# Optimization experiments

Measured on AMD Instinct MI355X. Metric: run time of the kernel, lower is better.

The kernel has to match this reference:

```python
import jax, jax.numpy as jnp
import numpy as np

B, S, D = 8, 1024, 2048
H, HD = 16, 128          # n_heads, head_dim (H*HD == D)
ROPE = 64                # rotary dims per head (front slice)
MAXB, MAXS = 10, 1024    # kv-cache buffer sizes (hardcoded in module)
START_POS = 0


def _apply_rope(x, cos_half, sin_half):
    # x: (BH, S, ROPE); cos/sin_half: (S, ROPE//2) -> tiled to (S, ROPE)
    cos_full = jnp.concatenate([cos_half, cos_half], axis=-1)
    sin_full = jnp.concatenate([sin_half, sin_half], axis=-1)
    half = x.shape[-1] // 2
    x1, x2 = x[..., :half], x[..., half:]
    rotated = jnp.concatenate([-x2, x1], axis=-1)
    return x * cos_full + rotated * sin_full


def setup_inputs() -> dict:
    key = jax.random.key(0)
    ks = jax.random.split(key, 6)
    sc = 0.02
    x = jax.random.normal(ks[0], (B, S, D), dtype=jnp.float32)
    wq = jax.random.normal(ks[1], (D, D), dtype=jnp.float32) * sc
    wk = jax.random.normal(ks[2], (D, D), dtype=jnp.float32) * sc
    wv = jax.random.normal(ks[3], (D, D), dtype=jnp.float32) * sc
    wo = jax.random.normal(ks[4], (D, D), dtype=jnp.float32) * sc
    bq = jnp.zeros((D,), jnp.float32)
    bk = jnp.zeros((D,), jnp.float32)
    bv = jnp.zeros((D,), jnp.float32)
    bo = jnp.zeros((D,), jnp.float32)
    # RoPE tables (HF "half" layout): angles over positions
    half = ROPE // 2
    inv_freq = 1.0 / (10000.0 ** (jnp.arange(half, dtype=jnp.float32) / half))
    ang = jnp.arange(S, dtype=jnp.float32)[:, None] * inv_freq[None, :]  # (S, half)
    cos_half = jnp.cos(ang)
    sin_half = jnp.sin(ang)
    mask = jnp.zeros((S, S), jnp.float32)  # additive mask, (seq, end_pos)
    cache_k = jnp.zeros((MAXB, MAXS, H * HD), jnp.float32)
    cache_v = jnp.zeros((MAXB, MAXS, H * HD), jnp.float32)
    return {
        "x": x, "wq": wq, "bq": bq, "wk": wk, "bk": bk, "wv": wv, "bv": bv,
        "wo": wo, "bo": bo, "cos_half": cos_half, "sin_half": sin_half,
        "mask": mask, "cache_k": cache_k, "cache_v": cache_v,
        "start_pos": START_POS,
    }


def reference(x, wq, bq, wk, bk, wv, bv, wo, bo, cos_half, sin_half, mask,
              cache_k, cache_v, start_pos):
    b, s, _ = x.shape
    end_pos = start_pos + s
    # QKV projections (torch Linear: y = x @ W.T + b)
    q = (x @ wq.T + bq).reshape(b, s, H, HD)
    k = (x @ wk.T + bk).reshape(b, s, H, HD)
    v = (x @ wv.T + bv).reshape(b, s, H, HD)
    # Partial RoPE on the first ROPE dims of each head
    q_head = q[..., :ROPE].transpose(0, 2, 1, 3).reshape(b * H, s, ROPE)
    k_head = k[..., :ROPE].transpose(0, 2, 1, 3).reshape(b * H, s, ROPE)
    q_head = _apply_rope(q_head, cos_half, sin_half)
    k_head = _apply_rope(k_head, cos_half, sin_half)
    q_head = q_head.reshape(b, H, s, ROPE).transpose(0, 2, 1, 3)
    k_head = k_head.reshape(b, H, s, ROPE).transpose(0, 2, 1, 3)
    q = jnp.concatenate([q_head, q[..., ROPE:]], axis=-1)
    k = jnp.concatenate([k_head, k[..., ROPE:]], axis=-1)
    # KV-cache write then read (start_pos is a static python int)
    cache_k = jax.lax.dynamic_update_slice(cache_k, k.reshape(b, s, H * HD), (0, start_pos, 0))
    cache_v = jax.lax.dynamic_update_slice(cache_v, v.reshape(b, s, H * HD), (0, start_pos, 0))
    k_cached = cache_k[:b, :end_pos].reshape(b, end_pos, H, HD)
    v_cached = cache_v[:b, :end_pos].reshape(b, end_pos, H, HD)
    # Unnormalized attention: no softmax, no scaling
    scores = jnp.einsum('bshd,bthd->bsht', q, k_cached)  # (B,S,H,T)
    scores = scores + mask[:, None, :]                   # (S,1,T) broadcast
    a_sum = jnp.einsum('bsht,bthd->bshd', scores, v_cached)
    out = a_sum.reshape(b, s, H * HD) @ wo.T + bo
    return out
```

## Files before the change

kernel.cpp:

```cpp
#include <hip/hip_runtime.h>
#include <stdint.h>

#define B_ 8
#define S_ 1024
#define D_ 2048
#define H_ 16
#define HD_ 128
#define NROW 8192
#define NQKV 6144

typedef __bf16 bf16;
typedef bf16  bf16x8 __attribute__((ext_vector_type(8)));
typedef bf16  bf16x4 __attribute__((ext_vector_type(4)));
typedef float f32x4  __attribute__((ext_vector_type(4)));

#define AS1 __attribute__((address_space(1)))
#define AS3 __attribute__((address_space(3)))

__device__ __forceinline__ void gl_lds16(const bf16* g, bf16* l) {
  __builtin_amdgcn_global_load_lds((AS1 void*)g, (AS3 void*)l, 16, 0, 0);
}

__global__ __launch_bounds__(256) void prep(const float* __restrict__ x,
                                            const float* __restrict__ wq,
                                            const float* __restrict__ wk,
                                            const float* __restrict__ wv,
                                            const float* __restrict__ wo,
                                            const float* __restrict__ mask,
                                            const float* __restrict__ bq,
                                            const float* __restrict__ bk,
                                            const float* __restrict__ bv,
                                            bf16* __restrict__ xb,
                                            bf16* __restrict__ wqkvb,
                                            bf16* __restrict__ wob,
                                            bf16* __restrict__ maskb,
                                            float* __restrict__ bqkv) {
  long i = (long)blockIdx.x * 256 + threadIdx.x;
  if (i < 8650752) {
    const float* src; bf16* dst; long j;
    if (i < 4194304)      { src = x;    dst = xb;              j = i; }
    else if (i < 5242880) { src = wq;   dst = wqkvb;           j = i - 4194304; }
    else if (i < 6291456) { src = wk;   dst = wqkvb + 4194304; j = i - 5242880; }
    else if (i < 7340032) { src = wv;   dst = wqkvb + 8388608; j = i - 6291456; }
    else if (i < 8388608) { src = wo;   dst = wob;             j = i - 7340032; }
    else                  { src = mask; dst = maskb;           j = i - 8388608; }
    float4 v = reinterpret_cast<const float4*>(src)[j];
    bf16x4 o;
    o.x = (bf16)v.x; o.y = (bf16)v.y; o.z = (bf16)v.z; o.w = (bf16)v.w;
    reinterpret_cast<bf16x4*>(dst)[j] = o;
  } else {
    long e = (i - 8650752) * 4;
    const float* s = (e < 2048) ? bq + e : (e < 4096 ? bk + (e - 2048) : bv + (e - 4096));
    *reinterpret_cast<float4*>(bqkv + e) = *reinterpret_cast<const float4*>(s);
  }
}

#define READ_A4(QA, KS, Ab)                                                   \
  _Pragma("unroll") for (int mi = 0; mi < 4; mi++)                            \
    af[mi] = *reinterpret_cast<const bf16x8*>(                                \
        (Ab) + aoff + ((((QA)*4 + mi)*2) + (KS))*512);

#define READ_B4(KS, Bb)                                                       \
  _Pragma("unroll") for (int ni = 0; ni < 4; ni++)                            \
    bfr[ni] = *reinterpret_cast<const bf16x8*>(                               \
        (Bb) + boff + ((ni*2) + (KS))*512);

#define MFMA16(QA)                                                            \
  _Pragma("unroll") for (int mi = 0; mi < 4; mi++)                            \
  _Pragma("unroll") for (int ni = 0; ni < 4; ni++)                            \
    acc[(QA)*4 + mi][ni] = __builtin_amdgcn_mfma_f32_16x16x32_bf16(           \
        af[mi], bfr[ni], acc[(QA)*4 + mi][ni], 0, 0, 0);

#define STAGE_H0(An, Bn, koff)                                                \
  gl_lds16(agA + (koff),           (An) + wid*1024);                          \
  gl_lds16(agA + 128*la + (koff),  (An) + (wid + 8)*1024);                    \
  gl_lds16(agB + (koff),           (Bn) + wid*1024);                          \
  gl_lds16(agB + 128*lb + (koff),  (Bn) + (wid + 8)*1024);

#define STAGE_H1(An, Bn, koff)                                                \
  gl_lds16(agA + (koff) + 32,          (An) + wid*1024 + 512);                \
  gl_lds16(agA + 128*la + (koff) + 32, (An) + (wid + 8)*1024 + 512);          \
  gl_lds16(agB + (koff) + 32,          (Bn) + wid*1024 + 512);                \
  gl_lds16(agB + 128*lb + (koff) + 32, (Bn) + (wid + 8)*1024 + 512);

#define GEMM256_MAIN_LOOP(NT)                                                 \
  { bf16* An = lds; bf16* Bn = lds + 16384;                                   \
    STAGE_H0(An, Bn, 0); STAGE_H1(An, Bn, 0); }                               \
  for (int t = 0; t < (NT); ++t) {                                            \
    const bf16* Ab = lds + (t & 1) * 32768;                                   \
    const bf16* Bb = Ab + 16384;                                              \
    bf16* An = lds + ((t & 1) ^ 1) * 32768;                                   \
    bf16* Bn = An + 16384;                                                    \
    const long kn = (long)(t + 1) * 64;                                       \
    const bool pf = (t + 1) < (NT);                                           \
    bf16x8 af[4], bfr[4];                                                     \
    asm volatile("s_waitcnt vmcnt(4)" ::: "memory");                          \
    __builtin_amdgcn_s_barrier();                                             \
    READ_A4(0, 0, Ab); READ_B4(0, Bb);                                        \
    if (pf) { STAGE_H0(An, Bn, kn); }                                         \
    asm volatile("s_waitcnt lgkmcnt(0)" ::: "memory");                        \
    __builtin_amdgcn_sched_barrier(0);                                        \
    __builtin_amdgcn_s_setprio(1); MFMA16(0); __builtin_amdgcn_s_setprio(0);  \
    READ_A4(1, 0, Ab);                                                        \
    asm volatile("s_waitcnt lgkmcnt(0)" ::: "memory");                        \
    __builtin_amdgcn_sched_barrier(0);                                        \
    __builtin_amdgcn_s_setprio(1); MFMA16(1); __builtin_amdgcn_s_setprio(0);  \
    if (pf) asm volatile("s_waitcnt vmcnt(4)" ::: "memory");                  \
    else    asm volatile("s_waitcnt vmcnt(0)" ::: "memory");                  \
    __builtin_amdgcn_s_barrier();                                             \
    READ_A4(0, 1, Ab); READ_B4(1, Bb);                                        \
    if (pf) { STAGE_H1(An, Bn, kn); }                                         \
    asm volatile("s_waitcnt lgkmcnt(0)" ::: "memory");                        \
    __builtin_amdgcn_sched_barrier(0);                                        \
    __builtin_amdgcn_s_setprio(1); MFMA16(0); __builtin_amdgcn_s_setprio(0);  \
    READ_A4(1, 1, Ab);                                                        \
    asm volatile("s_waitcnt lgkmcnt(0)" ::: "memory");                        \
    __builtin_amdgcn_sched_barrier(0);                                        \
    __builtin_amdgcn_s_setprio(1); MFMA16(1); __builtin_amdgcn_s_setprio(0);  \
  }

template <typename CT, bool BIAS, bool ACCUM, bool ROPE>
__global__ __launch_bounds__(512, 2) void gemm256(const bf16* __restrict__ A,
                                                  const bf16* __restrict__ Bm,
                                                  const float* __restrict__ bias,
                                                  CT* __restrict__ C,
                                                  int M, int N, int K,
                                                  long la, long lb, long lc,
                                                  long za, long zb, long zc,
                                                  const float* __restrict__ chp,
                                                  const float* __restrict__ shp) {
  extern __shared__ __align__(16) bf16 lds[];
  const int z = blockIdx.z;
  A  += (long)z * za;
  Bm += (long)z * zb;
  C  += (long)z * zc;
  const int tid  = threadIdx.x;
  const int wid  = tid >> 6;
  const int lane = tid & 63;
  const int wm0 = (wid >> 2) * 128;
  const int wn0 = (wid & 3) * 64;
  const int m0 = blockIdx.y * 256, n0 = blockIdx.x * 256;

  const int rr = lane >> 2;
  const int cc = ((lane & 3) * 8) ^ ((rr & 8) << 1);
  const bf16* agA = A  + (long)(m0 + wid * 16 + rr) * la + cc;
  const bf16* agB = Bm + (long)(n0 + wid * 16 + rr) * lb + cc;

  const int swz  = ((lane >> 4) * 8) ^ ((lane & 8) << 1);
  const int aoff = (wm0 >> 4) * 1024 + (lane & 15) * 32 + swz;
  const int boff = (wn0 >> 4) * 1024 + (lane & 15) * 32 + swz;

  f32x4 acc[8][4] = {};
  const int NT = K >> 6;

  GEMM256_MAIN_LOOP(NT);

#pragma unroll
  for (int mi = 0; mi < 8; mi++) {
    float vals[4][4];
#pragma unroll
    for (int ni = 0; ni < 4; ni++) {
      const int col = n0 + wn0 + ni * 16 + (lane & 15);
      float bv = 0.0f;
      if constexpr (BIAS) bv = bias[col];
#pragma unroll
      for (int r = 0; r < 4; r++) vals[ni][r] = acc[mi][ni][r] + bv;
    }
    if constexpr (ROPE) {
      if ((n0 + wn0) < 4096 && (((n0 + wn0) & 127) == 0)) {
#pragma unroll
        for (int ni = 0; ni < 2; ni++)
#pragma unroll
          for (int r = 0; r < 4; r++) {
            const int srow = (m0 + wm0 + mi * 16 + (lane >> 4) * 4 + r) & (S_ - 1);
            const int hd = ni * 16 + (lane & 15);
            const float c  = chp[srow * 32 + hd];
            const float sn = shp[srow * 32 + hd];
            const float a  = vals[ni][r], b2 = vals[ni + 2][r];
            vals[ni][r]     = a * c - b2 * sn;
            vals[ni + 2][r] = b2 * c + a * sn;
          }
      }
    }
#pragma unroll
    for (int ni = 0; ni < 4; ni++) {
      const int col = n0 + wn0 + ni * 16 + (lane & 15);
      const long base = (long)(m0 + wm0 + mi * 16 + (lane >> 4) * 4) * lc + col;
#pragma unroll
      for (int r = 0; r < 4; r++) {
        float v = vals[ni][r];
        if constexpr (ACCUM) v += (float)C[base + (long)r * lc];
        C[base + (long)r * lc] = (CT)v;
      }
    }
  }
}

__global__ __launch_bounds__(512, 2) void pv256(const bf16* __restrict__ Am,
                                                const bf16* __restrict__ Vt,
                                                const bf16* __restrict__ QKV,
                                                const bf16* __restrict__ W2,
                                                bf16* __restrict__ Ob) {
  extern __shared__ __align__(16) bf16 lds[];
  const int z = blockIdx.z;
  const bf16* A  = Am;
  const bf16* Bm = Vt + (long)z * (D_ * S_);
  bf16* C = Ob + (long)z * (S_ * D_);
  const long la = S_, lb = S_;
  const int tid  = threadIdx.x;
  const int wid  = tid >> 6;
  const int lane = tid & 63;
  const int wm0 = (wid >> 2) * 128;
  const int wn0 = (wid & 3) * 64;
  const int m0 = blockIdx.y * 256, n0 = blockIdx.x * 256;

  const int rr = lane >> 2;
  const int cc = ((lane & 3) * 8) ^ ((rr & 8) << 1);
  const bf16* agA = A  + (long)(m0 + wid * 16 + rr) * la + cc;
  const bf16* agB = Bm + (long)(n0 + wid * 16 + rr) * lb + cc;

  const int swz  = ((lane >> 4) * 8) ^ ((lane & 8) << 1);
  const int aoff = (wm0 >> 4) * 1024 + (lane & 15) * 32 + swz;
  const int boff = (wn0 >> 4) * 1024 + (lane & 15) * 32 + swz;

  f32x4 acc[8][4] = {};

  GEMM256_MAIN_LOOP(16);

  const int h0 = n0 >> 7;
  const int hsel = wn0 >> 7;
  const int a2base = hsel * 16384;
  const int b2base = 32768 + hsel * 8192;
  const int bsub = (wn0 & 64) >> 4;
  const int a2off = (wm0 >> 4) * 1024 + (lane & 15) * 32 + swz;
  const int b2off = (lane & 15) * 32 + swz;

#define STAGE_K2(e0)                                                          \
  { const bf16* qa0 = QKV + (long)(z * S_ + m0 + wid * 16 + rr) * NQKV        \
                      + h0 * 128 + (e0) + cc;                                 \
    gl_lds16(qa0,                       lds + wid * 1024);                    \
    gl_lds16(qa0 + 32,                  lds + wid * 1024 + 512);              \
    gl_lds16(qa0 + 128 * NQKV,          lds + (wid + 8) * 1024);              \
    gl_lds16(qa0 + 128 * NQKV + 32,     lds + (wid + 8) * 1024 + 512);        \
    gl_lds16(qa0 + 128,                 lds + 16384 + wid * 1024);            \
    gl_lds16(qa0 + 160,                 lds + 16384 + wid * 1024 + 512);      \
    gl_lds16(qa0 + 128 * NQKV + 128,    lds + 16384 + (wid + 8) * 1024);      \
    gl_lds16(qa0 + 128 * NQKV + 160,    lds + 16384 + (wid + 8) * 1024 + 512);\
    const bf16* w0 = W2 + (long)(z * 16 + h0) * 16384                         \
                     + (wid * 16 + rr) * 128 + (e0) + cc;                     \
    gl_lds16(w0,                        lds + 32768 + wid * 1024);            \
    gl_lds16(w0 + 32,                   lds + 32768 + wid * 1024 + 512);      \
    gl_lds16(w0 + 16384,                lds + 40960 + wid * 1024);            \
    gl_lds16(w0 + 16384 + 32,           lds + 40960 + wid * 1024 + 512);      }

  __builtin_amdgcn_s_barrier();
  STAGE_K2(0);
#pragma unroll
  for (int step = 0; step < 2; step++) {
    asm volatile("s_waitcnt vmcnt(0)" ::: "memory");
    __builtin_amdgcn_s_barrier();
    bf16x8 a2[8], b2[4];
#pragma unroll
    for (int ks = 0; ks < 2; ks++) {
#pragma unroll
      for (int mi = 0; mi < 8; mi++)
        a2[mi] = *reinterpret_cast<const bf16x8*>(
            lds + a2base + a2off + mi * 1024 + ks * 512);
#pragma unroll
      for (int ni = 0; ni < 4; ni++)
        b2[ni] = *reinterpret_cast<const bf16x8*>(
            lds + b2base + b2off + (bsub + ni) * 1024 + ks * 512);
      asm volatile("s_waitcnt lgkmcnt(0)" ::: "memory");
      __builtin_amdgcn_sched_barrier(0);
      __builtin_amdgcn_s_setprio(1);
#pragma unroll
      for (int mi = 0; mi < 8; mi++)
#pragma unroll
        for (int ni = 0; ni < 4; ni++)
          acc[mi][ni] = __builtin_amdgcn_mfma_f32_16x16x32_bf16(
              a2[mi], b2[ni], acc[mi][ni], 0, 0, 0);
      __builtin_amdgcn_s_setprio(0);
    }
    if (step == 0) {
      __builtin_amdgcn_s_barrier();
      STAGE_K2(64);
    }
  }
#undef STAGE_K2

#pragma unroll
  for (int mi = 0; mi < 8; mi++) {
#pragma unroll
    for (int ni = 0; ni < 4; ni++) {
      const int col = n0 + wn0 + ni * 16 + (lane & 15);
      const long base = (long)(m0 + wm0 + mi * 16 + (lane >> 4) * 4) * D_ + col;
#pragma unroll
      for (int r = 0; r < 4; r++)
        C[base + (long)r * D_] = (bf16)acc[mi][ni][r];
    }
  }
}

template <typename CT, bool BIAS, bool ACCUM>
__global__ __launch_bounds__(256) void gemm_bt(const bf16* __restrict__ A,
                                               const bf16* __restrict__ Bm,
                                               const float* __restrict__ bias,
                                               CT* __restrict__ C,
                                               int M, int N, int K,
                                               long la, long lb, long lc,
                                               long za, long zb, long zc) {
  __shared__ __align__(16) bf16 As[128 * 32];
  __shared__ __align__(16) bf16 Bs[128 * 32];
  const int z = blockIdx.z;
  A  += (long)z * za;
  Bm += (long)z * zb;
  C  += (long)z * zc;
  const int tid = threadIdx.x;
  const int w = tid >> 6, l = tid & 63;
  const int wm = (w & 1) * 64, wn = (w >> 1) * 64;
  const int m0 = blockIdx.y * 128, n0 = blockIdx.x * 128;
  const int lr = l & 15, lk = (l >> 4) * 8;
  const int er = (l >> 4) * 4;

  const bf16* ag = A  + (long)(m0 + (tid >> 2)) * la + (tid & 3) * 8;
  const bf16* bg = Bm + (long)(n0 + (tid >> 2)) * lb + (tid & 3) * 8;
  bf16* al = As + (w * 16) * 32;
  bf16* bl = Bs + (w * 16) * 32;

  f32x4 acc[4][4] = {};

  for (int k0 = 0; k0 < K; k0 += 32) {
    gl_lds16(ag + k0,            al);
    gl_lds16(ag + 64 * la + k0,  al + 64 * 32);
    gl_lds16(bg + k0,            bl);
    gl_lds16(bg + 64 * lb + k0,  bl + 64 * 32);
    __syncthreads();
    bf16x8 afr[4], bfr[4];
#pragma unroll
    for (int mi = 0; mi < 4; mi++)
      afr[mi] = *reinterpret_cast<const bf16x8*>(As + (wm + mi * 16 + lr) * 32 + lk);
#pragma unroll
    for (int ni = 0; ni < 4; ni++)
      bfr[ni] = *reinterpret_cast<const bf16x8*>(Bs + (wn + ni * 16 + lr) * 32 + lk);
#pragma unroll
    for (int mi = 0; mi < 4; mi++)
#pragma unroll
      for (int ni = 0; ni < 4; ni++)
        acc[mi][ni] = __builtin_amdgcn_mfma_f32_16x16x32_bf16(afr[mi], bfr[ni], acc[mi][ni], 0, 0, 0);
    __syncthreads();
  }

#pragma unroll
  for (int mi = 0; mi < 4; mi++) {
#pragma unroll
    for (int ni = 0; ni < 4; ni++) {
      const int col = n0 + wn + ni * 16 + lr;
      float bv = 0.0f;
      if constexpr (BIAS) bv = bias[col];
      const long base = (long)(m0 + wm + mi * 16 + er) * lc + col;
#pragma unroll
      for (int r = 0; r < 4; r++) {
        float v = acc[mi][ni][r] + bv;
        if constexpr (ACCUM) v += (float)C[base + (long)r * lc];
        C[base + (long)r * lc] = (CT)v;
      }
    }
  }
}

__global__ __launch_bounds__(256) void kvtrans(const bf16* __restrict__ QKV,
                                               bf16* __restrict__ Kt,
                                               bf16* __restrict__ Vt) {
  __shared__ unsigned short T[128 * 130];
  const int bid = blockIdx.x;
  const int tb = bid & 7, bh = (bid >> 3) & 127, kv = bid >> 10;
  const int b = bh >> 4, h = bh & 15;
  const int tid = threadIdx.x;
  const bf16* src = QKV + (long)(b * S_ + tb * 128) * NQKV + 2048 + kv * 2048 + h * HD_;
#pragma unroll
  for (int it = 0; it < 8; it++) {
    int chunk = it * 256 + tid;
    int r = chunk >> 4, hc = (chunk & 15) * 8;
    bf16x8 v = *reinterpret_cast<const bf16x8*>(src + (long)r * NQKV + hc);
    union { bf16x8 v8; unsigned short u[8]; } u8; u8.v8 = v;
#pragma unroll
    for (int j = 0; j < 8; j++) T[r * 130 + hc + j] = u8.u[j];
  }
  __syncthreads();
  bf16* dst = (kv ? Vt : Kt) + (long)bh * HD_ * S_ + tb * 128;
#pragma unroll
  for (int it = 0; it < 8; it++) {
    int chunk = it * 256 + tid;
    int hd = chunk >> 4, tc = (chunk & 15) * 8;
    union { bf16x8 v8; unsigned short u[8]; } u8;
#pragma unroll
    for (int j = 0; j < 8; j++) u8.u[j] = T[(tc + j) * 130 + hd];
    *reinterpret_cast<bf16x8*>(dst + (long)hd * S_ + tc) = u8.v8;
  }
}

extern "C" void kernel_launch(void* const* d_in, const int* in_sizes, int n_in,
                              void* d_out, int out_size, void* d_ws, size_t ws_size,
                              hipStream_t stream) {
  const float* x   = (const float*)d_in[0];
  const float* wq  = (const float*)d_in[1];
  const float* bq  = (const float*)d_in[2];
  const float* wk  = (const float*)d_in[3];
  const float* bk  = (const float*)d_in[4];
  const float* wv  = (const float*)d_in[5];
  const float* bv  = (const float*)d_in[6];
  const float* wo  = (const float*)d_in[7];
  const float* bo  = (const float*)d_in[8];
  const float* ch  = (const float*)d_in[9];
  const float* sh  = (const float*)d_in[10];
  const float* mask = (const float*)d_in[11];
  float* out = (float*)d_out;

  hipFuncSetAttribute(reinterpret_cast<const void*>(&gemm256<bf16, true, false, true>),
                      hipFuncAttributeMaxDynamicSharedMemorySize, 131072);
  hipFuncSetAttribute(reinterpret_cast<const void*>(&gemm256<float, true, false, false>),
                      hipFuncAttributeMaxDynamicSharedMemorySize, 131072);
  hipFuncSetAttribute(reinterpret_cast<const void*>(&pv256),
                      hipFuncAttributeMaxDynamicSharedMemorySize, 131072);

  char* ws = (char*)d_ws;
  bf16*  QKV   = (bf16*)(ws);
  bf16*  Vt    = (bf16*)(ws + 100663296);
  bf16*  Kt    = (bf16*)(ws + 134217728);
  bf16*  wob   = (bf16*)(ws + 167772160);
  float* bqkv  = (float*)(ws + 176160768);
  bf16*  maskb = (bf16*)(ws + 176185344);
  bf16*  W2    = (bf16*)(ws + 178282496);
  bf16*  Ob    = (bf16*)(ws + 182476800);
  bf16*  xb    = (bf16*)(ws + 216031232);
  bf16*  wqkvb = (bf16*)(ws + 249585664);

  prep<<<33798, 256, 0, stream>>>(x, wq, wk, wv, wo, mask, bq, bk, bv,
                                  xb, wqkvb, wob, maskb, bqkv);

  gemm256<bf16, true, false, true><<<dim3(24, 32, 1), 512, 131072, stream>>>(
      xb, wqkvb, bqkv, QKV, NROW, NQKV, D_,
      (long)D_, (long)D_, (long)NQKV, 0L, 0L, 0L, ch, sh);

  kvtrans<<<2048, 256, 0, stream>>>(QKV, Kt, Vt);

  gemm_bt<bf16, false, false><<<dim3(1, 1, 128), 256, 0, stream>>>(
      Vt, Kt, nullptr, W2, HD_, HD_, S_,
      (long)S_, (long)S_, (long)HD_,
      (long)(HD_ * S_), (long)(HD_ * S_), (long)(HD_ * HD_));

  pv256<<<dim3(8, 4, 8), 512, 131072, stream>>>(maskb, Vt, QKV, W2, Ob);

  gemm256<float, true, false, false><<<dim3(8, 32, 1), 512, 131072, stream>>>(
      Ob, wob, bo, out, NROW, D_, D_,
      (long)D_, (long)D_, (long)D_, 0L, 0L, 0L, nullptr, nullptr);
}
```

Before: 605.2 us.

## Fuse K/V transpose into QKV GEMM epilogue via LDS staging

The QKV projection GEMM epilogue now writes K and V tiles for columns at or above 2048 directly in transposed per-head layout (Kt/Vt). It stages them through swizzled LDS in two halves, which removes the separate kvtrans kernel launch. This avoids writing the K/V parts of QKV to global memory and reading them back for the transpose. The cost is extra LDS traffic and barriers in the GEMM epilogue, plus possible register pressure from the added template path.

```diff
diff --git a/kernel.cpp b/kernel.cpp
--- a/kernel.cpp
+++ b/kernel.cpp
@@ -119,7 +119,7 @@
     __builtin_amdgcn_s_setprio(1); MFMA16(1); __builtin_amdgcn_s_setprio(0);  \
   }
 
-template <typename CT, bool BIAS, bool ACCUM, bool ROPE>
+template <typename CT, bool BIAS, bool ACCUM, bool ROPE, int FUSE>
 __global__ __launch_bounds__(512, 2) void gemm256(const bf16* __restrict__ A,
                                                   const bf16* __restrict__ Bm,
                                                   const float* __restrict__ bias,
@@ -128,7 +128,9 @@
                                                   long la, long lb, long lc,
                                                   long za, long zb, long zc,
                                                   const float* __restrict__ chp,
-                                                  const float* __restrict__ shp) {
+                                                  const float* __restrict__ shp,
+                                                  bf16* __restrict__ Kt,
+                                                  bf16* __restrict__ Vt) {
   extern __shared__ __align__(16) bf16 lds[];
   const int z = blockIdx.z;
   A  += (long)z * za;
@@ -155,6 +157,72 @@
 
   GEMM256_MAIN_LOOP(NT);
 
+  const bool doRope = ROPE && (((n0 + wn0) & 127) == 0) && ((n0 + wn0) < 4096);
+
+  if (FUSE == 1 && n0 >= 2048) {
+    const int breg = m0 >> 10;
+    const int t0   = m0 & 1023;
+    const int relc = n0 & 2047;
+    bf16* XT = (n0 < 4096) ? Kt : Vt;
+    __builtin_amdgcn_s_barrier();
+#pragma unroll
+    for (int st = 0; st < 2; ++st) {
+#pragma unroll
+      for (int mi2 = 0; mi2 < 4; mi2++) {
+        const int mi = st * 4 + mi2;
+        float vals[4][4];
+#pragma unroll
+        for (int ni = 0; ni < 4; ni++) {
+          const int col = n0 + wn0 + ni * 16 + (lane & 15);
+          float bv = 0.0f;
+          if constexpr (BIAS) bv = bias[col];
+#pragma unroll
+          for (int r = 0; r < 4; r++) vals[ni][r] = acc[mi][ni][r] + bv;
+        }
+        if (doRope) {
+#pragma unroll
+          for (int ni = 0; ni < 2; ni++)
+#pragma unroll
+            for (int r = 0; r < 4; r++) {
+              const int srow = (m0 + wm0 + mi * 16 + (lane >> 4) * 4 + r) & (S_ - 1);
+              const int hd = ni * 16 + (lane & 15);
+              const float c  = chp[srow * 32 + hd];
+              const float sn = shp[srow * 32 + hd];
+              const float a  = vals[ni][r], b2 = vals[ni + 2][r];
+              vals[ni][r]     = a * c - b2 * sn;
+              vals[ni + 2][r] = b2 * c + a * sn;
+            }
+        }
+#pragma unroll
+        for (int ni = 0; ni < 4; ni++) {
+          const int col_l = wn0 + ni * 16 + (lane & 15);
+          const int row_l = wm0 + mi * 16 + ((lane >> 4) << 2);
+          const int pr = (row_l & 63) | ((row_l & 128) >> 1);
+          bf16x4 o;
+          o.x = (bf16)vals[ni][0]; o.y = (bf16)vals[ni][1];
+          o.z = (bf16)vals[ni][2]; o.w = (bf16)vals[ni][3];
+          *reinterpret_cast<bf16x4*>(
+              lds + col_l * 128 + (pr ^ ((col_l & 7) << 3))) = o;
+        }
+      }
+      __builtin_amdgcn_s_barrier();
+#pragma unroll
+      for (int it = 0; it < 8; ++it) {
+        const int idx = it * 512 + tid;
+        const int colg = idx >> 4;
+        const int tp8  = (idx & 15) * 8;
+        bf16x8 v = *reinterpret_cast<const bf16x8*>(
+            lds + colg * 128 + (tp8 ^ ((colg & 7) << 3)));
+        const int trow = (tp8 & 63) + ((tp8 >> 6) << 7) + st * 64;
+        const int bh = breg * 16 + (relc >> 7) + (colg >> 7);
+        *reinterpret_cast<bf16x8*>(
+            XT + (long)bh * (HD_ * S_) + (colg & 127) * S_ + t0 + trow) = v;
+      }
+      if (st == 0) __builtin_amdgcn_s_barrier();
+    }
+    return;
+  }
+
 #pragma unroll
   for (int mi = 0; mi < 8; mi++) {
     float vals[4][4];
@@ -167,7 +235,7 @@
       for (int r = 0; r < 4; r++) vals[ni][r] = acc[mi][ni][r] + bv;
     }
     if constexpr (ROPE) {
-      if ((n0 + wn0) < 4096 && (((n0 + wn0) & 127) == 0)) {
+      if (doRope) {
 #pragma unroll
         for (int ni = 0; ni < 2; ni++)
 #pragma unroll
@@ -368,37 +436,6 @@
   }
 }
 
-__global__ __launch_bounds__(256) void kvtrans(const bf16* __restrict__ QKV,
-                                               bf16* __restrict__ Kt,
-                                               bf16* __restrict__ Vt) {
-  __shared__ unsigned short T[128 * 130];
-  const int bid = blockIdx.x;
-  const int tb = bid & 7, bh = (bid >> 3) & 127, kv = bid >> 10;
-  const int b = bh >> 4, h = bh & 15;
-  const int tid = threadIdx.x;
-  const bf16* src = QKV + (long)(b * S_ + tb * 128) * NQKV + 2048 + kv * 2048 + h * HD_;
-#pragma unroll
-  for (int it = 0; it < 8; it++) {
-    int chunk = it * 256 + tid;
-    int r = chunk >> 4, hc = (chunk & 15) * 8;
-    bf16x8 v = *reinterpret_cast<const bf16x8*>(src + (long)r * NQKV + hc);
-    union { bf16x8 v8; unsigned short u[8]; } u8; u8.v8 = v;
-#pragma unroll
-    for (int j = 0; j < 8; j++) T[r * 130 + hc + j] = u8.u[j];
-  }
-  __syncthreads();
-  bf16* dst = (kv ? Vt : Kt) + (long)bh * HD_ * S_ + tb * 128;
-#pragma unroll
-  for (int it = 0; it < 8; it++) {
-    int chunk = it * 256 + tid;
-    int hd = chunk >> 4, tc = (chunk & 15) * 8;
-    union { bf16x8 v8; unsigned short u[8]; } u8;
-#pragma unroll
-    for (int j = 0; j < 8; j++) u8.u[j] = T[(tc + j) * 130 + hd];
-    *reinterpret_cast<bf16x8*>(dst + (long)hd * S_ + tc) = u8.v8;
-  }
-}
-
 extern "C" void kernel_launch(void* const* d_in, const int* in_sizes, int n_in,
                               void* d_out, int out_size, void* d_ws, size_t ws_size,
                               hipStream_t stream) {
@@ -416,9 +453,9 @@
   const float* mask = (const float*)d_in[11];
   float* out = (float*)d_out;
 
-  hipFuncSetAttribute(reinterpret_cast<const void*>(&gemm256<bf16, true, false, true>),
+  hipFuncSetAttribute(reinterpret_cast<const void*>(&gemm256<bf16, true, false, true, 1>),
                       hipFuncAttributeMaxDynamicSharedMemorySize, 131072);
-  hipFuncSetAttribute(reinterpret_cast<const void*>(&gemm256<float, true, false, false>),
+  hipFuncSetAttribute(reinterpret_cast<const void*>(&gemm256<float, true, false, false, 0>),
                       hipFuncAttributeMaxDynamicSharedMemorySize, 131072);
   hipFuncSetAttribute(reinterpret_cast<const void*>(&pv256),
                       hipFuncAttributeMaxDynamicSharedMemorySize, 131072);
@@ -438,11 +475,9 @@
   prep<<<33798, 256, 0, stream>>>(x, wq, wk, wv, wo, mask, bq, bk, bv,
                                   xb, wqkvb, wob, maskb, bqkv);
 
-  gemm256<bf16, true, false, true><<<dim3(24, 32, 1), 512, 131072, stream>>>(
+  gemm256<bf16, true, false, true, 1><<<dim3(24, 32, 1), 512, 131072, stream>>>(
       xb, wqkvb, bqkv, QKV, NROW, NQKV, D_,
-      (long)D_, (long)D_, (long)NQKV, 0L, 0L, 0L, ch, sh);
-
-  kvtrans<<<2048, 256, 0, stream>>>(QKV, Kt, Vt);
+      (long)D_, (long)D_, (long)NQKV, 0L, 0L, 0L, ch, sh, Kt, Vt);
 
   gemm_bt<bf16, false, false><<<dim3(1, 1, 128), 256, 0, stream>>>(
       Vt, Kt, nullptr, W2, HD_, HD_, S_,
@@ -451,7 +486,7 @@
 
   pv256<<<dim3(8, 4, 8), 512, 131072, stream>>>(maskb, Vt, QKV, W2, Ob);
 
-  gemm256<float, true, false, false><<<dim3(8, 32, 1), 512, 131072, stream>>>(
+  gemm256<float, true, false, false, 0><<<dim3(8, 32, 1), 512, 131072, stream>>>(
       Ob, wob, bo, out, NROW, D_, D_,
-      (long)D_, (long)D_, (long)D_, 0L, 0L, 0L, nullptr, nullptr);
-}
+      (long)D_, (long)D_, (long)D_, 0L, 0L, 0L, nullptr, nullptr, nullptr, nullptr);
+}
```

Result: faster. 568.2 us (-6.1%).
